# Performance work log

Hardware: AMD Instinct MI355X
Metric: run time of the kernel (lower is better)

Reference implementation:

```python
import jax, jax.numpy as jnp
import numpy as np

ANCHORS = np.array([[10.0, 13.0], [16.0, 30.0], [33.0, 23.0]], dtype=np.float32)
IMG_W, IMG_H = 416.0, 416.0
NUM_CLASSES = 80
NUM_ANCHORS = 3
IGNORE_THR = 0.5
LAMBDA_IOU, LAMBDA_CONF, LAMBDA_CLS = 0.5, 1.0, 1.0
EPS = 1e-7


def _bce(p, t):
    p = jnp.clip(p, EPS, 1.0 - EPS)
    return -(t * jnp.log(p) + (1.0 - t) * jnp.log(1.0 - p))


def _xywh_iou(x1, y1, w1, h1, x2, y2, w2, h2):
    iw = jnp.clip(jnp.minimum(x1 + w1 * 0.5, x2 + w2 * 0.5) - jnp.maximum(x1 - w1 * 0.5, x2 - w2 * 0.5), 0.0)
    ih = jnp.clip(jnp.minimum(y1 + h1 * 0.5, y2 + h2 * 0.5) - jnp.maximum(y1 - h1 * 0.5, y2 - h2 * 0.5), 0.0)
    inter = iw * ih
    return inter / (w1 * h1 + w2 * h2 - inter + 1e-16)


def _decode(targets, anchors, in_w, in_h):
    # Vectorized version of the per-target python loop. Scatter with
    # out-of-bounds indices (default 'drop' mode) skips invalid/empty targets.
    B, T = targets.shape[0], targets.shape[1]
    A = anchors.shape[0]
    valid = jnp.sum(targets, axis=-1) != 0  # [B,T]
    gx = targets[..., 1] * in_w
    gy = targets[..., 2] * in_h
    gw = targets[..., 3] * in_w
    gh = targets[..., 4] * in_h
    gi = gx.astype(jnp.int32)
    gj = gy.astype(jnp.int32)
    cls = targets[..., 0].astype(jnp.int32)
    aw, ah = anchors[:, 0], anchors[:, 1]
    # anchor-vs-gt IoU at origin (center format): [B,T,A]
    inter = jnp.minimum(gw[..., None], aw) * jnp.minimum(gh[..., None], ah)
    anch_iou = inter / (gw[..., None] * gh[..., None] + aw * ah - inter + 1e-16)
    best_n = jnp.argmax(anch_iou, axis=-1)  # [B,T]
    gi_s = jnp.where(valid, gi, in_w)  # invalid -> OOB -> dropped
    gj_s = jnp.where(valid, gj, in_h)
    bb = jnp.broadcast_to(jnp.arange(B)[:, None], (B, T))
    shape = (B, A, in_h, in_w)
    zeros = jnp.zeros(shape, jnp.float32)
    # noobj: zero out every anchor with IoU > thr at the gt cell
    bb3 = jnp.broadcast_to(jnp.arange(B)[:, None, None], (B, T, A))
    aa3 = jnp.broadcast_to(jnp.arange(A)[None, None, :], (B, T, A))
    gj3 = jnp.broadcast_to(gj_s[..., None], (B, T, A))
    gi3 = jnp.broadcast_to(gi_s[..., None], (B, T, A))
    noobj = jnp.ones(shape, jnp.float32).at[bb3, aa3, gj3, gi3].min(
        jnp.where(anch_iou > IGNORE_THR, 0.0, 1.0))
    scat = lambda v: zeros.at[bb, best_n, gj_s, gi_s].set(v)
    mask = zeros.at[bb, best_n, gj_s, gi_s].max(jnp.ones_like(gx))
    tx = scat(gx - gi.astype(jnp.float32))
    ty = scat(gy - gj.astype(jnp.float32))
    tw = scat(jnp.log(gw / aw[best_n] + 1e-16))
    th = scat(jnp.log(gh / ah[best_n] + 1e-16))
    kx, ky, kw, kh = scat(gx), scat(gy), scat(gw), scat(gh)
    tconf = mask
    tcls = jnp.zeros(shape + (NUM_CLASSES,), jnp.float32).at[bb, best_n, gj_s, gi_s, cls].set(1.0)
    return mask, noobj, tx, ty, tw, th, kx, ky, kw, kh, tconf, tcls


def reference(input, targets):
    bs, _, in_h, in_w = input.shape
    stride_h = IMG_H / in_h
    stride_w = IMG_W / in_w
    scaled = jnp.asarray(ANCHORS) / jnp.array([stride_w, stride_h], jnp.float32)  # [A,2]
    pred = input.reshape(bs, NUM_ANCHORS, 5 + NUM_CLASSES, in_h, in_w).transpose(0, 1, 3, 4, 2)
    x = jax.nn.sigmoid(pred[..., 0])
    y = jax.nn.sigmoid(pred[..., 1])
    w = pred[..., 2]
    h = pred[..., 3]
    conf = jax.nn.sigmoid(pred[..., 4])
    pred_cls = jax.nn.sigmoid(pred[..., 5:])
    dec = _decode(targets, scaled, in_w, in_h)
    # targets in torch are requires_grad=False buffers -> constants
    mask, noobj, tx, ty, tw, th, kx, ky, kw, kh, tconf, tcls = [jax.lax.stop_gradient(t) for t in dec]
    grid_x = jnp.arange(in_w, dtype=jnp.float32)[None, None, None, :]
    grid_y = jnp.arange(in_h, dtype=jnp.float32)[None, None, :, None]
    anchor_w = scaled[:, 0][None, :, None, None]
    anchor_h = scaled[:, 1][None, :, None, None]
    # torch uses x.data / w.data -> detached box decode, no grad through IoU loss
    hx = jax.lax.stop_gradient(x) + grid_x
    hy = jax.lax.stop_gradient(y) + grid_y
    hw = jnp.exp(jax.lax.stop_gradient(w)) * anchor_w
    hh = jnp.exp(jax.lax.stop_gradient(h)) * anchor_h
    iou = _xywh_iou(hx, hy, hw, hh, kx, ky, kw, kh)
    loss_iou = jnp.sum((1.0 - iou) * mask)
    loss_conf = jnp.mean(_bce(conf * mask, mask)) + 0.5 * jnp.mean(_bce(conf * noobj, jnp.zeros_like(noobj)))
    n_pos = jnp.maximum(jnp.sum(mask), 1.0)
    # BCELoss mean over the mask==1 positions only (n_pos * C elements)
    loss_cls = jnp.sum(_bce(pred_cls, tcls) * mask[..., None]) / (n_pos * NUM_CLASSES)
    loss = loss_iou * LAMBDA_IOU + loss_conf * LAMBDA_CONF + loss_cls * LAMBDA_CLS
    return loss, loss_iou, loss_conf, loss_cls


def setup_inputs() -> dict:
    key = jax.random.key(0)
    k1, k2, k3, k4 = jax.random.split(key, 4)
    B, T = 32, 50
    inp = jax.random.normal(k1, (B, 255, 52, 52), dtype=jnp.float32) * 0.5
    cls = jnp.floor(jax.random.uniform(k2, (B, T, 1)) * NUM_CLASSES)
    xy = jax.random.uniform(k3, (B, T, 2), minval=0.02, maxval=0.98)
    wh = jax.random.uniform(k4, (B, T, 2), minval=0.05, maxval=0.30)
    targets = jnp.concatenate([cls, xy, wh], axis=-1).astype(jnp.float32)
    return {"input": inp, "targets": targets}
```

## Files before the change

kernel.cpp:

```cpp
#include <hip/hip_runtime.h>
#include <stdint.h>

#define BATCH 32
#define NA 3
#define GH 52
#define GW 52
#define NT 50
#define NCLS 80
#define HW_ (GH * GW)
#define NCELL (BATCH * NA * HW_)
#define NBA (BATCH * NA)
#define CQUAD (HW_ / 4)
#define NBLKA NBA
#define NCHUNK 4
#define CHUNK 13
#define NBLKB (BATCH * NCHUNK)
#define NPART (NBLKA + NBLKB)
#define POISON 0xAAAAAAAAu
#define CEPS 1.0000000494e-07f

__device__ __forceinline__ float sp(float z) {
    return fmaxf(z, 0.f) + log1pf(expf(-fabsf(z)));
}
__device__ __forceinline__ float sigmf(float x) { return 1.f / (1.f + expf(-x)); }

__device__ __forceinline__ float wred(float v) {
    #pragma unroll
    for (int o = 32; o > 0; o >>= 1) v += __shfl_down(v, o, 64);
    return v;
}

__global__ __launch_bounds__(256) void k_all(const float* __restrict__ in,
                                             const float* __restrict__ tg,
                                             float* __restrict__ part,
                                             uint32_t* __restrict__ cnt,
                                             float* __restrict__ out) {
    __shared__ float red[4][5];
    __shared__ bool  is_last;
    const int bid = blockIdx.x, tid = threadIdx.x;
    float s0 = 0.f, s1 = 0.f, s2 = 0.f, s3 = 0.f, s4 = 0.f;

    if (bid < NBLKA) {
        const float4* cp = reinterpret_cast<const float4*>(
            in + ((size_t)(bid * 85 + 4)) * HW_);
        #pragma unroll
        for (int k = 0; k < 3; ++k) {
            int q = tid + k * 256;
            if (q < CQUAD) {
                float4 v = cp[q];
                s2 += sp(v.x) + sp(v.y) + sp(v.z) + sp(v.w);
            }
        }
    } else {
        __shared__ int      sinfo[NT];
        __shared__ float4   sbox[NT];
        __shared__ int      plist_info[CHUNK];
        __shared__ float4   plist_box[CHUNK];
        __shared__ uint32_t plist_c[CHUNK][3];
        __shared__ int      nolist[3 * CHUNK];
        __shared__ int      pcnt[2];

        const int pb = bid - NBLKA;
        const int b  = pb >> 2;
        const int ch = pb & 3;
        if (tid == 0) { pcnt[0] = 0; pcnt[1] = 0; }

        if (tid < NT) {
            const float* p = tg + (b * NT + tid) * 5;
            float f0 = p[0], f1 = p[1], f2 = p[2], f3 = p[3], f4 = p[4];
            int info = 0;
            float gx = f1 * GW, gy = f2 * GH, gw = f3 * GW, gh = f4 * GH;
            int gi = (int)gx, gj = (int)gy, cls = (int)f0;
            bool valid = (f0 + f1 + f2 + f3 + f4) != 0.0f &&
                         gi >= 0 && gi < GW && gj >= 0 && gj < GH;
            if (valid) {
                const float aw0 = 1.25f, aw1 = 2.0f, aw2 = 4.125f;
                const float ah0 = 1.625f, ah1 = 3.75f, ah2 = 2.875f;
                float ga = gw * gh;
                float i0 = fminf(gw, aw0) * fminf(gh, ah0); float u0 = i0 / (ga + aw0 * ah0 - i0 + 1e-16f);
                float i1 = fminf(gw, aw1) * fminf(gh, ah1); float u1 = i1 / (ga + aw1 * ah1 - i1 + 1e-16f);
                float i2 = fminf(gw, aw2) * fminf(gh, ah2); float u2 = i2 / (ga + aw2 * ah2 - i2 + 1e-16f);
                int bn = 0; float best = u0;
                if (u1 > best) { best = u1; bn = 1; }
                if (u2 > best) { best = u2; bn = 2; }
                int thr = (u0 > 0.5f ? 1 : 0) | (u1 > 0.5f ? 2 : 0) | (u2 > 0.5f ? 4 : 0);
                int clp = cls < 0 ? 0 : (cls > 127 ? 127 : cls);
                info = gi | (gj << 6) | (bn << 12) | (thr << 14) | (1 << 17) | (clp << 18)
                       | ((cls >= 0 && cls < NCLS) ? (1 << 25) : 0);
                sbox[tid] = make_float4(gx, gy, gw, gh);
            }
            sinfo[tid] = info;
        }
        __syncthreads();

        if (tid < CHUNK) {
            int t = ch * CHUNK + tid;
            if (t < NT) {
                int inf = sinfo[t];
                if (inf & (1 << 17)) {
                    int key = inf & 0x3FFF;
                    bool owner = true;
                    for (int t2 = t + 1; t2 < NT; ++t2) {
                        int i2 = sinfo[t2];
                        if ((i2 & (1 << 17)) && ((i2 & 0x3FFF) == key)) { owner = false; break; }
                    }
                    if (owner) {
                        uint32_t c0 = 0, c1 = 0, c2 = 0;
                        for (int t2 = 0; t2 < NT; ++t2) {
                            int i2 = sinfo[t2];
                            if ((i2 & (1 << 17)) && ((i2 & 0x3FFF) == key) && (i2 & (1 << 25))) {
                                int cl = (i2 >> 18) & 127;
                                if (cl < 32)      c0 |= 1u << cl;
                                else if (cl < 64) c1 |= 1u << (cl - 32);
                                else if (cl < NCLS) c2 |= 1u << (cl - 64);
                            }
                        }
                        int slot = atomicAdd(&pcnt[0], 1);
                        plist_info[slot] = inf; plist_box[slot] = sbox[t];
                        plist_c[slot][0] = c0; plist_c[slot][1] = c1; plist_c[slot][2] = c2;
                    }
                }
            }
        }
        if (tid < 3 * CHUNK) {
            int t = ch * CHUNK + tid / 3, a = tid % 3;
            if (t < NT) {
                int inf = sinfo[t];
                if ((inf & (1 << 17)) && ((inf >> (14 + a)) & 1)) {
                    bool owner = true;
                    for (int t2 = 0; t2 < t; ++t2) {
                        int i2 = sinfo[t2];
                        if ((i2 & (1 << 17)) && ((i2 & 0xFFF) == (inf & 0xFFF)) &&
                            ((i2 >> (14 + a)) & 1)) { owner = false; break; }
                    }
                    if (owner) {
                        int slot = atomicAdd(&pcnt[1], 1);
                        nolist[slot] = (inf & 0xFFF) | (a << 12);
                    }
                }
            }
        }
        __syncthreads();

        const int wv = tid >> 6, lane = tid & 63;
        const int npos = pcnt[0], nno = pcnt[1];

        for (int c = wv; c < npos; c += 4) {
            int inf = plist_info[c];
            int gi = inf & 63, gj = (inf >> 6) & 63, bn = (inf >> 12) & 3;
            const float* base = in + ((size_t)((b * NA + bn) * 85)) * HW_ + (gj * GW + gi);
            float v0 = base[lane * HW_];
            float v1 = (lane < 21) ? base[(64 + lane) * HW_] : 0.f;
            float z0 = __shfl(v0, 0, 64), z1 = __shfl(v0, 1, 64);
            float z2 = __shfl(v0, 2, 64), z3 = __shfl(v0, 3, 64);
            float z4 = __shfl(v0, 4, 64);
            float aw = (bn == 0) ? 1.25f  : (bn == 1) ? 2.0f  : 4.125f;
            float ah = (bn == 0) ? 1.625f : (bn == 1) ? 3.75f : 2.875f;
            float hx = sigmf(z0) + (float)gi, hy = sigmf(z1) + (float)gj;
            float hw = expf(z2) * aw,         hh = expf(z3) * ah;
            float4 bx = plist_box[c];
            float iw = fmaxf(fminf(hx + hw * .5f, bx.x + bx.z * .5f) -
                             fmaxf(hx - hw * .5f, bx.x - bx.z * .5f), 0.f);
            float ih = fmaxf(fminf(hy + hh * .5f, bx.y + bx.w * .5f) -
                             fmaxf(hy - hh * .5f, bx.y - bx.w * .5f), 0.f);
            float inter = iw * ih;
            float iou = inter / (hw * hh + bx.z * bx.w - inter + 1e-16f);
            uint32_t c0 = plist_c[c][0], c1 = plist_c[c][1], c2 = plist_c[c][2];
            float contrib = 0.f;
            if (lane >= 5) {
                int cl = lane - 5;
                uint32_t bit = (cl < 32) ? ((c0 >> cl) & 1u)
                             : (cl < 64) ? ((c1 >> (cl - 32)) & 1u)
                                         : ((c2 >> (cl - 64)) & 1u);
                contrib += bit ? sp(-v0) : sp(v0);
            }
            if (lane < 21) {
                int cl = 59 + lane;
                uint32_t bit = (cl < 64) ? ((c1 >> (cl - 32)) & 1u)
                                         : ((c2 >> (cl - 64)) & 1u);
                contrib += bit ? sp(-v1) : sp(v1);
            }
            float tot = wred(contrib);
            if (lane == 0) {
                s3 += tot;
                s0 += 1.0f - iou;
                s1 += sp(-z4) - CEPS;
                s4 += 1.0f;
            }
        }
        for (int k = tid; k < nno; k += 256) {
            int e = nolist[k];
            int gi = e & 63, gj = (e >> 6) & 63, a = e >> 12;
            float z = in[((size_t)((b * NA + a) * 85 + 4)) * HW_ + (gj * GW + gi)];
            s2 += CEPS - sp(z);
        }
    }

    s0 = wred(s0); s1 = wred(s1); s2 = wred(s2); s3 = wred(s3); s4 = wred(s4);
    const int wv2 = tid >> 6;
    if ((tid & 63) == 0) {
        red[wv2][0] = s0; red[wv2][1] = s1; red[wv2][2] = s2;
        red[wv2][3] = s3; red[wv2][4] = s4;
    }
    __syncthreads();
    if (tid == 0) {
        float a0 = 0, a1 = 0, a2 = 0, a3 = 0, a4 = 0;
        #pragma unroll
        for (int w = 0; w < 4; ++w) {
            a0 += red[w][0]; a1 += red[w][1]; a2 += red[w][2];
            a3 += red[w][3]; a4 += red[w][4];
        }
        float* pp = part + (size_t)bid * 5;
        pp[0] = a0; pp[1] = a1; pp[2] = a2; pp[3] = a3; pp[4] = a4;
        __threadfence();
        uint32_t old = atomicAdd(cnt, 1u);
        is_last = (old == (uint32_t)(POISON + (NPART - 1)));
    }
    __syncthreads();

    if (is_last) {
        __threadfence();
        float t0 = 0, t1 = 0, t2 = 0, t3 = 0, t4 = 0;
        if (tid < NPART) {
            const volatile float* pp = part + (size_t)tid * 5;
            t0 = pp[0]; t1 = pp[1]; t2 = pp[2]; t3 = pp[3]; t4 = pp[4];
        }
        t0 = wred(t0); t1 = wred(t1); t2 = wred(t2); t3 = wred(t3); t4 = wred(t4);
        if ((tid & 63) == 0) {
            red[wv2][0] = t0; red[wv2][1] = t1; red[wv2][2] = t2;
            red[wv2][3] = t3; red[wv2][4] = t4;
        }
        __syncthreads();
        if (tid == 0) {
            float a0 = 0, a1 = 0, a2 = 0, a3 = 0, a4 = 0;
            #pragma unroll
            for (int w = 0; w < 4; ++w) {
                a0 += red[w][0]; a1 += red[w][1]; a2 += red[w][2];
                a3 += red[w][3]; a4 += red[w][4];
            }
            const float N = (float)NCELL;
            float loss_iou  = a0;
            float loss_conf = ((float)NCELL * CEPS + a1) / N + 0.5f * (a2 / N);
            float npos      = fmaxf(a4, 1.0f);
            float loss_cls  = a3 / (npos * (float)NCLS);
            float loss = 0.5f * loss_iou + loss_conf + loss_cls;
            out[0] = loss; out[1] = loss_iou; out[2] = loss_conf; out[3] = loss_cls;
        }
    }
}

extern "C" void kernel_launch(void* const* d_in, const int* in_sizes, int n_in,
                              void* d_out, int out_size, void* d_ws, size_t ws_size,
                              hipStream_t stream) {
    const float* input   = (const float*)d_in[0];
    const float* targets = (const float*)d_in[1];
    float* out = (float*)d_out;

    float*    part = (float*)d_ws;
    uint32_t* cnt  = (uint32_t*)((char*)d_ws + 8192);

    k_all<<<NPART, 256, 0, stream>>>(input, targets, part, cnt, out);
}
```

Before: 135.2 us.

## Prefetch positive-cell gathers before ownership pass and split final reduction kernel

Each wave now issues its strided gathers of the 85 channel values for candidate targets before the ownership/class-bitmask scan, so those latencies overlap the shared-memory dedup work instead of following a barrier. Ownership is recorded per slot rather than compacted with atomics, and the per-target warp reduction of class loss is deferred into the per-thread accumulator. The last-block atomic counter scheme (which relied on a poison-initialized workspace) is replaced by a separate one-block final reduction kernel, adding a launch but removing the fence and atomic.

```diff
diff --git a/kernel.cpp b/kernel.cpp
--- a/kernel.cpp
+++ b/kernel.cpp
@@ -13,10 +13,9 @@
 #define CQUAD (HW_ / 4)
 #define NBLKA NBA
 #define NCHUNK 4
-#define CHUNK 13
+#define CHN 13
 #define NBLKB (BATCH * NCHUNK)
 #define NPART (NBLKA + NBLKB)
-#define POISON 0xAAAAAAAAu
 #define CEPS 1.0000000494e-07f
 
 __device__ __forceinline__ float sp(float z) {
@@ -30,13 +29,10 @@
     return v;
 }
 
-__global__ __launch_bounds__(256) void k_all(const float* __restrict__ in,
-                                             const float* __restrict__ tg,
-                                             float* __restrict__ part,
-                                             uint32_t* __restrict__ cnt,
-                                             float* __restrict__ out) {
+__global__ __launch_bounds__(256) void k_main(const float* __restrict__ in,
+                                              const float* __restrict__ tg,
+                                              float* __restrict__ part) {
     __shared__ float red[4][5];
-    __shared__ bool  is_last;
     const int bid = blockIdx.x, tid = threadIdx.x;
     float s0 = 0.f, s1 = 0.f, s2 = 0.f, s3 = 0.f, s4 = 0.f;
 
@@ -54,16 +50,15 @@
     } else {
         __shared__ int      sinfo[NT];
         __shared__ float4   sbox[NT];
-        __shared__ int      plist_info[CHUNK];
-        __shared__ float4   plist_box[CHUNK];
-        __shared__ uint32_t plist_c[CHUNK][3];
-        __shared__ int      nolist[3 * CHUNK];
-        __shared__ int      pcnt[2];
+        __shared__ int      sown[CHN];
+        __shared__ uint32_t scls[CHN][3];
+        __shared__ int      nolist[3 * CHN];
+        __shared__ int      ncnt;
 
         const int pb = bid - NBLKA;
         const int b  = pb >> 2;
         const int ch = pb & 3;
-        if (tid == 0) { pcnt[0] = 0; pcnt[1] = 0; }
+        if (tid == 0) ncnt = 0;
 
         if (tid < NT) {
             const float* p = tg + (b * NT + tid) * 5;
@@ -93,19 +88,42 @@
         }
         __syncthreads();
 
-        if (tid < CHUNK) {
-            int t = ch * CHUNK + tid;
+        const int wv = tid >> 6, lane = tid & 63;
+
+        float v0[4], v1[4];
+        int   tgt[4];
+        bool  cand[4];
+        #pragma unroll
+        for (int k = 0; k < 4; ++k) {
+            int idx = wv + 4 * k;
+            int t   = ch * CHN + idx;
+            cand[k] = false; tgt[k] = 0; v0[k] = 0.f; v1[k] = 0.f;
+            if (idx < CHN && t < NT) {
+                int inf = sinfo[t];
+                if (inf & (1 << 17)) {
+                    cand[k] = true; tgt[k] = t;
+                    int gi = inf & 63, gj = (inf >> 6) & 63, bn = (inf >> 12) & 3;
+                    const float* base = in + ((size_t)((b * NA + bn) * 85)) * HW_
+                                           + (gj * GW + gi);
+                    v0[k] = base[lane * HW_];
+                    v1[k] = (lane < 21) ? base[(64 + lane) * HW_] : 0.f;
+                }
+            }
+        }
+
+        if (tid < CHN) {
+            int t = ch * CHN + tid;
+            int own = 0; uint32_t c0 = 0, c1 = 0, c2 = 0;
             if (t < NT) {
                 int inf = sinfo[t];
                 if (inf & (1 << 17)) {
                     int key = inf & 0x3FFF;
-                    bool owner = true;
+                    own = 1;
                     for (int t2 = t + 1; t2 < NT; ++t2) {
                         int i2 = sinfo[t2];
-                        if ((i2 & (1 << 17)) && ((i2 & 0x3FFF) == key)) { owner = false; break; }
-                    }
-                    if (owner) {
-                        uint32_t c0 = 0, c1 = 0, c2 = 0;
+                        if ((i2 & (1 << 17)) && ((i2 & 0x3FFF) == key)) { own = 0; break; }
+                    }
+                    if (own) {
                         for (int t2 = 0; t2 < NT; ++t2) {
                             int i2 = sinfo[t2];
                             if ((i2 & (1 << 17)) && ((i2 & 0x3FFF) == key) && (i2 & (1 << 25))) {
@@ -115,15 +133,15 @@
                                 else if (cl < NCLS) c2 |= 1u << (cl - 64);
                             }
                         }
-                        int slot = atomicAdd(&pcnt[0], 1);
-                        plist_info[slot] = inf; plist_box[slot] = sbox[t];
-                        plist_c[slot][0] = c0; plist_c[slot][1] = c1; plist_c[slot][2] = c2;
-                    }
-                }
-            }
-        }
-        if (tid < 3 * CHUNK) {
-            int t = ch * CHUNK + tid / 3, a = tid % 3;
+                    }
+                }
+            }
+            sown[tid] = own;
+            scls[tid][0] = c0; scls[tid][1] = c1; scls[tid][2] = c2;
+        }
+        if (tid < 3 * CHN) {
+            int idx = tid / 3, a = tid % 3;
+            int t = ch * CHN + idx;
             if (t < NT) {
                 int inf = sinfo[t];
                 if ((inf & (1 << 17)) && ((inf >> (14 + a)) & 1)) {
@@ -134,7 +152,7 @@
                             ((i2 >> (14 + a)) & 1)) { owner = false; break; }
                     }
                     if (owner) {
-                        int slot = atomicAdd(&pcnt[1], 1);
+                        int slot = atomicAdd(&ncnt, 1);
                         nolist[slot] = (inf & 0xFFF) | (a << 12);
                     }
                 }
@@ -142,54 +160,52 @@
         }
         __syncthreads();
 
-        const int wv = tid >> 6, lane = tid & 63;
-        const int npos = pcnt[0], nno = pcnt[1];
-
-        for (int c = wv; c < npos; c += 4) {
-            int inf = plist_info[c];
-            int gi = inf & 63, gj = (inf >> 6) & 63, bn = (inf >> 12) & 3;
-            const float* base = in + ((size_t)((b * NA + bn) * 85)) * HW_ + (gj * GW + gi);
-            float v0 = base[lane * HW_];
-            float v1 = (lane < 21) ? base[(64 + lane) * HW_] : 0.f;
-            float z0 = __shfl(v0, 0, 64), z1 = __shfl(v0, 1, 64);
-            float z2 = __shfl(v0, 2, 64), z3 = __shfl(v0, 3, 64);
-            float z4 = __shfl(v0, 4, 64);
-            float aw = (bn == 0) ? 1.25f  : (bn == 1) ? 2.0f  : 4.125f;
-            float ah = (bn == 0) ? 1.625f : (bn == 1) ? 3.75f : 2.875f;
-            float hx = sigmf(z0) + (float)gi, hy = sigmf(z1) + (float)gj;
-            float hw = expf(z2) * aw,         hh = expf(z3) * ah;
-            float4 bx = plist_box[c];
-            float iw = fmaxf(fminf(hx + hw * .5f, bx.x + bx.z * .5f) -
-                             fmaxf(hx - hw * .5f, bx.x - bx.z * .5f), 0.f);
-            float ih = fmaxf(fminf(hy + hh * .5f, bx.y + bx.w * .5f) -
-                             fmaxf(hy - hh * .5f, bx.y - bx.w * .5f), 0.f);
-            float inter = iw * ih;
-            float iou = inter / (hw * hh + bx.z * bx.w - inter + 1e-16f);
-            uint32_t c0 = plist_c[c][0], c1 = plist_c[c][1], c2 = plist_c[c][2];
-            float contrib = 0.f;
-            if (lane >= 5) {
-                int cl = lane - 5;
-                uint32_t bit = (cl < 32) ? ((c0 >> cl) & 1u)
-                             : (cl < 64) ? ((c1 >> (cl - 32)) & 1u)
-                                         : ((c2 >> (cl - 64)) & 1u);
-                contrib += bit ? sp(-v0) : sp(v0);
-            }
-            if (lane < 21) {
-                int cl = 59 + lane;
-                uint32_t bit = (cl < 64) ? ((c1 >> (cl - 32)) & 1u)
-                                         : ((c2 >> (cl - 64)) & 1u);
-                contrib += bit ? sp(-v1) : sp(v1);
-            }
-            float tot = wred(contrib);
-            if (lane == 0) {
-                s3 += tot;
-                s0 += 1.0f - iou;
-                s1 += sp(-z4) - CEPS;
-                s4 += 1.0f;
-            }
-        }
-        for (int k = tid; k < nno; k += 256) {
-            int e = nolist[k];
+        #pragma unroll
+        for (int k = 0; k < 4; ++k) {
+            int idx = wv + 4 * k;
+            if (cand[k] && idx < CHN && sown[idx]) {
+                int t = tgt[k];
+                int inf = sinfo[t];
+                int gi = inf & 63, gj = (inf >> 6) & 63, bn = (inf >> 12) & 3;
+                float z0 = __shfl(v0[k], 0, 64), z1 = __shfl(v0[k], 1, 64);
+                float z2 = __shfl(v0[k], 2, 64), z3 = __shfl(v0[k], 3, 64);
+                float z4 = __shfl(v0[k], 4, 64);
+                float aw = (bn == 0) ? 1.25f  : (bn == 1) ? 2.0f  : 4.125f;
+                float ah = (bn == 0) ? 1.625f : (bn == 1) ? 3.75f : 2.875f;
+                float hx = sigmf(z0) + (float)gi, hy = sigmf(z1) + (float)gj;
+                float hw = expf(z2) * aw,         hh = expf(z3) * ah;
+                float4 bx = sbox[t];
+                float iw = fmaxf(fminf(hx + hw * .5f, bx.x + bx.z * .5f) -
+                                 fmaxf(hx - hw * .5f, bx.x - bx.z * .5f), 0.f);
+                float ih = fmaxf(fminf(hy + hh * .5f, bx.y + bx.w * .5f) -
+                                 fmaxf(hy - hh * .5f, bx.y - bx.w * .5f), 0.f);
+                float inter = iw * ih;
+                float iou = inter / (hw * hh + bx.z * bx.w - inter + 1e-16f);
+                uint32_t c0 = scls[idx][0], c1 = scls[idx][1], c2 = scls[idx][2];
+                float contrib = 0.f;
+                if (lane >= 5) {
+                    int cl = lane - 5;
+                    uint32_t bit = (cl < 32) ? ((c0 >> cl) & 1u)
+                                 : (cl < 64) ? ((c1 >> (cl - 32)) & 1u)
+                                             : ((c2 >> (cl - 64)) & 1u);
+                    contrib += bit ? sp(-v0[k]) : sp(v0[k]);
+                }
+                if (lane < 21) {
+                    int cl = 59 + lane;
+                    uint32_t bit = (cl < 64) ? ((c1 >> (cl - 32)) & 1u)
+                                             : ((c2 >> (cl - 64)) & 1u);
+                    contrib += bit ? sp(-v1[k]) : sp(v1[k]);
+                }
+                s3 += contrib;
+                if (lane == 0) {
+                    s0 += 1.0f - iou;
+                    s1 += sp(-z4) - CEPS;
+                    s4 += 1.0f;
+                }
+            }
+        }
+        for (int k2 = tid; k2 < ncnt; k2 += 256) {
+            int e = nolist[k2];
             int gi = e & 63, gj = (e >> 6) & 63, a = e >> 12;
             float z = in[((size_t)((b * NA + a) * 85 + 4)) * HW_ + (gj * GW + gi)];
             s2 += CEPS - sp(z);
@@ -212,40 +228,39 @@
         }
         float* pp = part + (size_t)bid * 5;
         pp[0] = a0; pp[1] = a1; pp[2] = a2; pp[3] = a3; pp[4] = a4;
-        __threadfence();
-        uint32_t old = atomicAdd(cnt, 1u);
-        is_last = (old == (uint32_t)(POISON + (NPART - 1)));
+    }
+}
+
+__global__ __launch_bounds__(256) void k_final(const float* __restrict__ part,
+                                               float* __restrict__ out) {
+    __shared__ float red[4][5];
+    int tid = threadIdx.x;
+    float s0 = 0, s1 = 0, s2 = 0, s3 = 0, s4 = 0;
+    if (tid < NPART) {
+        const float* pp = part + (size_t)tid * 5;
+        s0 = pp[0]; s1 = pp[1]; s2 = pp[2]; s3 = pp[3]; s4 = pp[4];
+    }
+    s0 = wred(s0); s1 = wred(s1); s2 = wred(s2); s3 = wred(s3); s4 = wred(s4);
+    int wv = tid >> 6;
+    if ((tid & 63) == 0) {
+        red[wv][0] = s0; red[wv][1] = s1; red[wv][2] = s2;
+        red[wv][3] = s3; red[wv][4] = s4;
     }
     __syncthreads();
-
-    if (is_last) {
-        __threadfence();
-        float t0 = 0, t1 = 0, t2 = 0, t3 = 0, t4 = 0;
-        if (tid < NPART) {
-            const volatile float* pp = part + (size_t)tid * 5;
-            t0 = pp[0]; t1 = pp[1]; t2 = pp[2]; t3 = pp[3]; t4 = pp[4];
-        }
-        t0 = wred(t0); t1 = wred(t1); t2 = wred(t2); t3 = wred(t3); t4 = wred(t4);
-        if ((tid & 63) == 0) {
-            red[wv2][0] = t0; red[wv2][1] = t1; red[wv2][2] = t2;
-            red[wv2][3] = t3; red[wv2][4] = t4;
-        }
-        __syncthreads();
-        if (tid == 0) {
-            float a0 = 0, a1 = 0, a2 = 0, a3 = 0, a4 = 0;
-            #pragma unroll
-            for (int w = 0; w < 4; ++w) {
-                a0 += red[w][0]; a1 += red[w][1]; a2 += red[w][2];
-                a3 += red[w][3]; a4 += red[w][4];
-            }
-            const float N = (float)NCELL;
-            float loss_iou  = a0;
-            float loss_conf = ((float)NCELL * CEPS + a1) / N + 0.5f * (a2 / N);
-            float npos      = fmaxf(a4, 1.0f);
-            float loss_cls  = a3 / (npos * (float)NCLS);
-            float loss = 0.5f * loss_iou + loss_conf + loss_cls;
-            out[0] = loss; out[1] = loss_iou; out[2] = loss_conf; out[3] = loss_cls;
-        }
+    if (tid == 0) {
+        float a0 = 0, a1 = 0, a2 = 0, a3 = 0, a4 = 0;
+        #pragma unroll
+        for (int w = 0; w < 4; ++w) {
+            a0 += red[w][0]; a1 += red[w][1]; a2 += red[w][2];
+            a3 += red[w][3]; a4 += red[w][4];
+        }
+        const float N = (float)NCELL;
+        float loss_iou  = a0;
+        float loss_conf = ((float)NCELL * CEPS + a1) / N + 0.5f * (a2 / N);
+        float npos      = fmaxf(a4, 1.0f);
+        float loss_cls  = a3 / (npos * (float)NCLS);
+        float loss = 0.5f * loss_iou + loss_conf + loss_cls;
+        out[0] = loss; out[1] = loss_iou; out[2] = loss_conf; out[3] = loss_cls;
     }
 }
 
@@ -254,10 +269,9 @@
                               hipStream_t stream) {
     const float* input   = (const float*)d_in[0];
     const float* targets = (const float*)d_in[1];
-    float* out = (float*)d_out;
-
-    float*    part = (float*)d_ws;
-    uint32_t* cnt  = (uint32_t*)((char*)d_ws + 8192);
-
-    k_all<<<NPART, 256, 0, stream>>>(input, targets, part, cnt, out);
-}
+    float* out  = (float*)d_out;
+    float* part = (float*)d_ws;
+
+    k_main <<<NPART, 256, 0, stream>>>(input, targets, part);
+    k_final<<<1, 256, 0, stream>>>(part, out);
+}
```

New measurement: 132.5 us. 2.0% less time.
